# Optimization experiments

Measured on AMD Instinct MI355X. Metric: run time of the kernel, lower is better.

Reference implementation:

```python
import jax, jax.numpy as jnp
import numpy as np

N, C, H, M = 4096, 1024, 16, 4096
D = C // H
EPS = 1e-6


def rms_norm(x, g):
    # RMSNorm32: normalize in fp32 with eps=1e-6, affine scale g
    x32 = x.astype(jnp.float32)
    inv = jax.lax.rsqrt(jnp.mean(x32 * x32, axis=-1, keepdims=True) + EPS)
    return (x32 * inv).astype(x.dtype) * g


def setup_inputs() -> dict:
    key = jax.random.key(0)
    ks = jax.random.split(key, 6)
    s = 1.0 / np.sqrt(C)
    return {
        "x": jax.random.normal(ks[0], (N, C), jnp.float32),
        "g1": jnp.ones((C,), jnp.float32),
        "g2": jnp.ones((C,), jnp.float32),
        "w_qkv": jax.random.normal(ks[1], (C, 3 * C), jnp.float32) * s,
        "w_o": jax.random.normal(ks[2], (C, C), jnp.float32) * s,
        "w1": jax.random.normal(ks[3], (C, M), jnp.float32) * s,
        "w2": jax.random.normal(ks[4], (M, C), jnp.float32) * (1.0 / np.sqrt(M)),
    }


def reference(x, g1, g2, w_qkv, w_o, w1, w2):
    # --- pre-norm + full multi-head self-attention over all N sparse tokens ---
    h = rms_norm(x, g1)                                   # [N, C]
    qkv = (h @ w_qkv).reshape(N, 3, H, D)                 # [N, 3, H, D]
    q, k, v = qkv[:, 0], qkv[:, 1], qkv[:, 2]             # [N, H, D]
    scale = 1.0 / np.sqrt(D)
    scores = jnp.einsum('nhd,mhd->hnm', q, k) * scale     # [H, N, N]
    attn = jax.nn.softmax(scores, axis=-1)
    o = jnp.einsum('hnm,mhd->nhd', attn, v).reshape(N, C) # [N, C]
    x = x + o @ w_o                                       # residual
    # --- pre-norm + gated-free MLP (GELU tanh) ---
    h2 = rms_norm(x, g2)
    m = jax.nn.gelu(h2 @ w1, approximate=True) @ w2       # [N, C]
    return x + m
```

## Files before the change

### kernel.cpp

```cpp
#include <hip/hip_runtime.h>
#include <stdint.h>

#define TOK 4096
#define CH  1024
#define NH  16
#define HD  64
#define FF  4096

typedef __attribute__((ext_vector_type(8))) short bf16x8;
typedef __attribute__((ext_vector_type(4))) float f32x4;
typedef __attribute__((ext_vector_type(16))) float f32x16;

__device__ __forceinline__ unsigned short f2bf(float f) {
    union { float f; unsigned u; } v; v.f = f;
    unsigned u = v.u;
    u += 0x7fffu + ((u >> 16) & 1u);
    return (unsigned short)(u >> 16);
}

__device__ __forceinline__ unsigned cvtpk(float a, float b) {
    unsigned r;
    asm("v_cvt_pk_bf16_f32 %0, %1, %2" : "=v"(r) : "v"(a), "v"(b));
    return r;
}

__device__ __forceinline__ void load_lds16(const void* g, void* l) {
    __builtin_amdgcn_global_load_lds(
        (const __attribute__((address_space(1))) unsigned int*)g,
        (__attribute__((address_space(3))) unsigned int*)l, 16, 0, 0);
}

__device__ __forceinline__ float gelu_tanh(float u) {
    float z = 0.7978845608028654f * (u + 0.044715f * u * u * u);
    float e = __expf(2.0f * z);
    return 0.5f * u * (1.0f + (1.0f - 2.0f / (e + 1.0f)));
}

__global__ __launch_bounds__(256) void wT_kernel(const float* __restrict__ in,
                                                 unsigned short* __restrict__ out,
                                                 int K, int Nn) {
    __shared__ float tile[32][33];
    int k0 = blockIdx.x * 32, n0 = blockIdx.y * 32;
    int t = threadIdx.x, r = t >> 3, c = t & 7;
#pragma unroll
    for (int i = 0; i < 4; i++)
        tile[r][c + 8 * i] = in[(size_t)(k0 + r) * Nn + n0 + c + 8 * i];
    __syncthreads();
#pragma unroll
    for (int i = 0; i < 4; i++)
        out[(size_t)(n0 + r) * K + k0 + c + 8 * i] = f2bf(tile[c + 8 * i][r]);
}

__global__ __launch_bounds__(256) void rms_kernel(const float* __restrict__ x,
                                                  const float* __restrict__ g,
                                                  unsigned short* __restrict__ out) {
    int row = blockIdx.x, t = threadIdx.x;
    const float4* xr = (const float4*)(x + (size_t)row * CH);
    float4 v = xr[t];
    float ss = v.x * v.x + v.y * v.y + v.z * v.z + v.w * v.w;
#pragma unroll
    for (int m = 32; m; m >>= 1) ss += __shfl_xor(ss, m, 64);
    __shared__ float wsum[4];
    if ((t & 63) == 0) wsum[t >> 6] = ss;
    __syncthreads();
    float inv = rsqrtf((wsum[0] + wsum[1] + wsum[2] + wsum[3]) * (1.0f / CH) + 1e-6f);
    float4 gv = ((const float4*)g)[t];
    ushort4 o;
    o.x = f2bf(v.x * inv * gv.x);
    o.y = f2bf(v.y * inv * gv.y);
    o.z = f2bf(v.z * inv * gv.z);
    o.w = f2bf(v.w * inv * gv.w);
    ((ushort4*)(out + (size_t)row * CH))[t] = o;
}

template<int EPI>
__global__ __launch_bounds__(256) void gemm_bt(const unsigned short* __restrict__ A,
                                               const unsigned short* __restrict__ Bt,
                                               void* __restrict__ outp,
                                               const float* __restrict__ resid,
                                               int M, int Nn, int K) {
    __shared__ __align__(16) unsigned short lds[2][2][128 * 32];
    const int t = threadIdx.x, l = t & 63, w = t >> 6;
    const int nbn = Nn >> 7;
    const int bid = blockIdx.x, nwg = gridDim.x, cpx = nwg >> 3;
    const int swz = (bid & 7) * cpx + (bid >> 3);
    const int bm = swz / nbn, bn = swz % nbn;
    const int wr = w >> 1, wc = w & 1;
    const unsigned short* Ag = A + (size_t)bm * 128 * K;
    const unsigned short* Bg = Bt + (size_t)bn * 128 * K;

    f32x4 acc[4][4];
#pragma unroll
    for (int m = 0; m < 4; m++)
#pragma unroll
        for (int n = 0; n < 4; n++) acc[m][n] = {0.f, 0.f, 0.f, 0.f};

    auto stage = [&](int buf, int kt) {
#pragma unroll
        for (int p = 0; p < 2; p++) {
            int c = t + 256 * p;
            load_lds16(Ag + (size_t)(c >> 2) * K + kt * 32 + (c & 3) * 8, &lds[buf][0][c * 8]);
        }
#pragma unroll
        for (int p = 0; p < 2; p++) {
            int c = t + 256 * p;
            load_lds16(Bg + (size_t)(c >> 2) * K + kt * 32 + (c & 3) * 8, &lds[buf][1][c * 8]);
        }
    };

    stage(0, 0);
    __syncthreads();
    const int nkt = K >> 5;
    for (int kt = 0; kt < nkt; kt++) {
        const int buf = kt & 1;
        if (kt + 1 < nkt) stage(buf ^ 1, kt + 1);
        bf16x8 af[4], bfr[4];
#pragma unroll
        for (int m = 0; m < 4; m++)
            af[m] = *(const bf16x8*)&lds[buf][0][(wr * 64 + m * 16 + (l & 15)) * 32 + (l >> 4) * 8];
#pragma unroll
        for (int n = 0; n < 4; n++)
            bfr[n] = *(const bf16x8*)&lds[buf][1][(wc * 64 + n * 16 + (l & 15)) * 32 + (l >> 4) * 8];
#pragma unroll
        for (int m = 0; m < 4; m++)
#pragma unroll
            for (int n = 0; n < 4; n++)
                acc[m][n] = __builtin_amdgcn_mfma_f32_16x16x32_bf16(af[m], bfr[n], acc[m][n], 0, 0, 0);
        __syncthreads();
    }

    const int r0 = bm * 128 + wr * 64, c0 = bn * 128 + wc * 64;
#pragma unroll
    for (int m = 0; m < 4; m++)
#pragma unroll
        for (int n = 0; n < 4; n++)
#pragma unroll
            for (int r = 0; r < 4; r++) {
                int rr = r0 + m * 16 + (l >> 4) * 4 + r;
                int cc = c0 + n * 16 + (l & 15);
                float v = acc[m][n][r];
                if (EPI == 0) {
                    ((unsigned short*)outp)[(size_t)rr * Nn + cc] = f2bf(v);
                } else if (EPI == 1) {
                    ((unsigned short*)outp)[(size_t)rr * Nn + cc] = f2bf(gelu_tanh(v));
                } else if (EPI == 3) {
                    float sc = (cc < 1024) ? 0.180336880f : 1.0f;
                    ((unsigned short*)outp)[(size_t)rr * Nn + cc] = f2bf(v * sc);
                } else {
                    ((float*)outp)[(size_t)rr * Nn + cc] = resid[(size_t)rr * Nn + cc] + v;
                }
            }
}

__global__ __launch_bounds__(256) void vT_kernel(const unsigned short* __restrict__ qkv,
                                                 unsigned short* __restrict__ vT) {
    __shared__ unsigned short tile[64][80];
    const int t = threadIdx.x;
    const int t0 = blockIdx.x * 64;
    const int h = blockIdx.y;
#pragma unroll
    for (int p = 0; p < 2; p++) {
        int c = t + 256 * p;
        int r = c >> 3, c8 = (c & 7) * 8;
        bf16x8 v = *(const bf16x8*)(qkv + (size_t)(t0 + r) * 3072 + 2048 + h * 64 + c8);
        *(bf16x8*)&tile[r][c8] = v;
    }
    __syncthreads();
#pragma unroll
    for (int p = 0; p < 2; p++) {
        int c = t + 256 * p;
        int col = c >> 3, r8 = (c & 7) * 8;
        union { unsigned short u[8]; bf16x8 v; } o;
#pragma unroll
        for (int j = 0; j < 8; j++) o.u[j] = tile[r8 + j][col];
        *(bf16x8*)(vT + (size_t)(h * 64 + col) * 4096 + t0 + r8) = o.v;
    }
}

__global__ __launch_bounds__(256) void attn_kernel(const unsigned short* __restrict__ qkv,
                                                   const unsigned short* __restrict__ vT,
                                                   unsigned short* __restrict__ o) {
    __shared__ __align__(16) unsigned short Kl[2][4096];
    __shared__ __align__(16) unsigned short Vl[2][4096];
    const int t = threadIdx.x, l = t & 63, w = t >> 6;
    const int h = blockIdx.y;
    const int qrow = blockIdx.x * 128 + w * 32 + (l & 31);

    bf16x8 qf[4];
    {
        const unsigned short* qp = qkv + (size_t)qrow * 3072 + h * 64 + ((l >> 5) * 8);
#pragma unroll
        for (int c = 0; c < 4; c++) qf[c] = *(const bf16x8*)(qp + 16 * c);
    }
    const unsigned short* kb = qkv + 1024 + h * 64;
    const unsigned short* vb = vT + (size_t)h * 64 * 4096;

    int off8[4];
#pragma unroll
    for (int c = 0; c < 4; c++)
        off8[c] = (l & 31) * 64 + ((((l >> 5) + 2 * c) ^ (l & 7)) * 8);
    int kst[2], vst[2];
#pragma unroll
    for (int p = 0; p < 2; p++) {
        int c = t + 256 * p;
        int r = c >> 3, b = c & 7;
        kst[p] = r * 3072 + ((b ^ (r & 7)) * 8);
        vst[p] = r * 4096 + ((b ^ (r & 7)) * 8);
    }

    float lrun = 0.f;
    f32x16 accO[2];
#pragma unroll
    for (int dt = 0; dt < 2; dt++)
#pragma unroll
        for (int i = 0; i < 16; i++) accO[dt][i] = 0.f;

    auto stage = [&](int buf, int kt) {
#pragma unroll
        for (int p = 0; p < 2; p++)
            load_lds16(kb + (size_t)kt * 64 * 3072 + kst[p], &Kl[buf][(t + 256 * p) * 8]);
#pragma unroll
        for (int p = 0; p < 2; p++)
            load_lds16(vb + kt * 64 + vst[p], &Vl[buf][(t + 256 * p) * 8]);
    };

    stage(0, 0);
    __syncthreads();

    for (int kt = 0; kt < 64; kt++) {
        const int cur = kt & 1;
        if (kt + 1 < 64) stage(cur ^ 1, kt + 1);

        f32x16 s[2];
#pragma unroll
        for (int st = 0; st < 2; st++)
#pragma unroll
            for (int i = 0; i < 16; i++) s[st][i] = 0.f;

        __builtin_amdgcn_s_setprio(1);
#pragma unroll
        for (int st = 0; st < 2; st++)
#pragma unroll
            for (int c = 0; c < 4; c++) {
                bf16x8 kf = *(const bf16x8*)&Kl[cur][st * 2048 + off8[c]];
                s[st] = __builtin_amdgcn_mfma_f32_32x32x16_bf16(kf, qf[c], s[st], 0, 0, 0);
            }
        __builtin_amdgcn_s_setprio(0);

        float rs = 0.f;
#pragma unroll
        for (int st = 0; st < 2; st++)
#pragma unroll
            for (int i = 0; i < 16; i++) {
                float p = __builtin_amdgcn_exp2f(s[st][i]);
                s[st][i] = p;
                rs += p;
            }
        lrun += rs;

#pragma unroll
        for (int kc = 0; kc < 4; kc++) {
            const int base = 8 * (kc & 1);
            const f32x16& S = s[kc >> 1];
            unsigned w0 = cvtpk(S[base + 0], S[base + 1]);
            unsigned w1 = cvtpk(S[base + 2], S[base + 3]);
            unsigned w2 = cvtpk(S[base + 4], S[base + 5]);
            unsigned w3 = cvtpk(S[base + 6], S[base + 7]);
            asm("v_permlane32_swap_b32 %0, %1" : "+v"(w0), "+v"(w2));
            asm("v_permlane32_swap_b32 %0, %1" : "+v"(w1), "+v"(w3));
            union { unsigned u[4]; bf16x8 v; } pf;
            pf.u[0] = w0; pf.u[1] = w1; pf.u[2] = w2; pf.u[3] = w3;
            __builtin_amdgcn_s_setprio(1);
#pragma unroll
            for (int dt = 0; dt < 2; dt++) {
                bf16x8 vf = *(const bf16x8*)&Vl[cur][dt * 2048 + off8[kc]];
                accO[dt] = __builtin_amdgcn_mfma_f32_32x32x16_bf16(vf, pf.v, accO[dt], 0, 0, 0);
            }
            __builtin_amdgcn_s_setprio(0);
        }
        __syncthreads();
    }

    lrun += __shfl_xor(lrun, 32, 64);
    float inv = 1.0f / lrun;
    unsigned short* ob = o + (size_t)qrow * CH + h * 64 + 4 * (l >> 5);
#pragma unroll
    for (int dt = 0; dt < 2; dt++)
#pragma unroll
        for (int qd = 0; qd < 4; qd++) {
            ushort4 pk;
            pk.x = f2bf(accO[dt][qd * 4 + 0] * inv);
            pk.y = f2bf(accO[dt][qd * 4 + 1] * inv);
            pk.z = f2bf(accO[dt][qd * 4 + 2] * inv);
            pk.w = f2bf(accO[dt][qd * 4 + 3] * inv);
            *(ushort4*)(ob + dt * 32 + qd * 8) = pk;
        }
}

extern "C" void kernel_launch(void* const* d_in, const int* in_sizes, int n_in,
                              void* d_out, int out_size, void* d_ws, size_t ws_size,
                              hipStream_t stream) {
    const float* x     = (const float*)d_in[0];
    const float* g1    = (const float*)d_in[1];
    const float* g2    = (const float*)d_in[2];
    const float* w_qkv = (const float*)d_in[3];
    const float* w_o   = (const float*)d_in[4];
    const float* w1    = (const float*)d_in[5];
    const float* w2    = (const float*)d_in[6];

    char* ws = (char*)d_ws;
    unsigned short* wqkvT = (unsigned short*)(ws);
    unsigned short* woT   = (unsigned short*)(ws + 6291456);
    unsigned short* w1T   = (unsigned short*)(ws + 8388608);
    unsigned short* w2T   = (unsigned short*)(ws + 16777216);
    unsigned short* hbuf  = (unsigned short*)(ws + 25165824);
    unsigned short* qkv   = (unsigned short*)(ws + 33554432);
    unsigned short* obuf  = (unsigned short*)(ws + 58720256);
    float*          x2    = (float*)(ws + 67108864);
    unsigned short* abuf  = (unsigned short*)(ws + 83886080);
    unsigned short* vTb   = (unsigned short*)(ws + 83886080);

    dim3 b256(256);
    wT_kernel<<<dim3(CH / 32, 3 * CH / 32), b256, 0, stream>>>(w_qkv, wqkvT, CH, 3 * CH);
    wT_kernel<<<dim3(CH / 32, CH / 32),     b256, 0, stream>>>(w_o,   woT,   CH, CH);
    wT_kernel<<<dim3(CH / 32, FF / 32),     b256, 0, stream>>>(w1,    w1T,   CH, FF);
    wT_kernel<<<dim3(FF / 32, CH / 32),     b256, 0, stream>>>(w2,    w2T,   FF, CH);

    rms_kernel<<<TOK, b256, 0, stream>>>(x, g1, hbuf);
    gemm_bt<3><<<(TOK / 128) * (3 * CH / 128), b256, 0, stream>>>(hbuf, wqkvT, qkv, nullptr, TOK, 3 * CH, CH);
    vT_kernel<<<dim3(TOK / 64, NH), b256, 0, stream>>>(qkv, vTb);
    attn_kernel<<<dim3(TOK / 128, NH), b256, 0, stream>>>(qkv, vTb, obuf);
    gemm_bt<2><<<(TOK / 128) * (CH / 128), b256, 0, stream>>>(obuf, woT, x2, x, TOK, CH, CH);
    rms_kernel<<<TOK, b256, 0, stream>>>(x2, g2, hbuf);
    gemm_bt<1><<<(TOK / 128) * (FF / 128), b256, 0, stream>>>(hbuf, w1T, abuf, nullptr, TOK, FF, CH);
    gemm_bt<2><<<(TOK / 128) * (CH / 128), b256, 0, stream>>>(abuf, w2T, (float*)d_out, x2, TOK, CH, FF);
}
```

Baseline: 312.7 us.

## Split attention key range across wave pairs and read V fragments directly

The attention block now covers 64 queries instead of 128. Its four waves form two query halves times two key halves, each wave pair processing 32 of the 64 key tiles, and the partial outputs and row sums are merged through LDS at the end. This doubles the grid size, which helps occupancy and load balance. V is no longer staged in LDS; each wave loads its V fragments straight from global memory (transposed vT) into registers, removing the V LDS traffic. The cost is more global and L2 traffic for K and V per query, plus an extra reduction step.

```diff
diff --git a/kernel.cpp b/kernel.cpp
--- a/kernel.cpp
+++ b/kernel.cpp
@@ -180,11 +180,11 @@
 __global__ __launch_bounds__(256) void attn_kernel(const unsigned short* __restrict__ qkv,
                                                    const unsigned short* __restrict__ vT,
                                                    unsigned short* __restrict__ o) {
-    __shared__ __align__(16) unsigned short Kl[2][4096];
-    __shared__ __align__(16) unsigned short Vl[2][4096];
+    __shared__ __align__(16) unsigned short Kl[2][2][4096];
     const int t = threadIdx.x, l = t & 63, w = t >> 6;
     const int h = blockIdx.y;
-    const int qrow = blockIdx.x * 128 + w * 32 + (l & 31);
+    const int qhalf = w & 1, kthalf = w >> 1;
+    const int qrow = blockIdx.x * 64 + qhalf * 32 + (l & 31);
 
     bf16x8 qf[4];
     {
@@ -193,19 +193,19 @@
         for (int c = 0; c < 4; c++) qf[c] = *(const bf16x8*)(qp + 16 * c);
     }
     const unsigned short* kb = qkv + 1024 + h * 64;
-    const unsigned short* vb = vT + (size_t)h * 64 * 4096;
+    const unsigned short* vrow = vT + (size_t)(h * 64 + (l & 31)) * 4096 + (l >> 5) * 8;
 
     int off8[4];
 #pragma unroll
     for (int c = 0; c < 4; c++)
         off8[c] = (l & 31) * 64 + ((((l >> 5) + 2 * c) ^ (l & 7)) * 8);
-    int kst[2], vst[2];
-#pragma unroll
-    for (int p = 0; p < 2; p++) {
-        int c = t + 256 * p;
+    int kst[4], ldst[4];
+#pragma unroll
+    for (int p = 0; p < 4; p++) {
+        int c = qhalf * 64 + l + 128 * p;
         int r = c >> 3, b = c & 7;
         kst[p] = r * 3072 + ((b ^ (r & 7)) * 8);
-        vst[p] = r * 4096 + ((b ^ (r & 7)) * 8);
+        ldst[p] = c * 8;
     }
 
     float lrun = 0.f;
@@ -215,34 +215,32 @@
 #pragma unroll
         for (int i = 0; i < 16; i++) accO[dt][i] = 0.f;
 
-    auto stage = [&](int buf, int kt) {
-#pragma unroll
-        for (int p = 0; p < 2; p++)
-            load_lds16(kb + (size_t)kt * 64 * 3072 + kst[p], &Kl[buf][(t + 256 * p) * 8]);
-#pragma unroll
-        for (int p = 0; p < 2; p++)
-            load_lds16(vb + kt * 64 + vst[p], &Vl[buf][(t + 256 * p) * 8]);
+    auto stageK = [&](int buf, int ktg) {
+#pragma unroll
+        for (int p = 0; p < 4; p++)
+            load_lds16(kb + (size_t)ktg * 64 * 3072 + kst[p], &Kl[kthalf][buf][ldst[p]]);
     };
 
-    stage(0, 0);
-    __syncthreads();
-
-    for (int kt = 0; kt < 64; kt++) {
-        const int cur = kt & 1;
-        if (kt + 1 < 64) stage(cur ^ 1, kt + 1);
+    const int kt0 = kthalf * 32;
+    stageK(0, kt0);
+    __syncthreads();
+
+    for (int i = 0; i < 32; i++) {
+        const int cur = i & 1;
+        if (i + 1 < 32) stageK(cur ^ 1, kt0 + i + 1);
 
         f32x16 s[2];
 #pragma unroll
         for (int st = 0; st < 2; st++)
 #pragma unroll
-            for (int i = 0; i < 16; i++) s[st][i] = 0.f;
+            for (int j = 0; j < 16; j++) s[st][j] = 0.f;
 
         __builtin_amdgcn_s_setprio(1);
 #pragma unroll
         for (int st = 0; st < 2; st++)
 #pragma unroll
             for (int c = 0; c < 4; c++) {
-                bf16x8 kf = *(const bf16x8*)&Kl[cur][st * 2048 + off8[c]];
+                bf16x8 kf = *(const bf16x8*)&Kl[kthalf][cur][st * 2048 + off8[c]];
                 s[st] = __builtin_amdgcn_mfma_f32_32x32x16_bf16(kf, qf[c], s[st], 0, 0, 0);
             }
         __builtin_amdgcn_s_setprio(0);
@@ -251,13 +249,22 @@
 #pragma unroll
         for (int st = 0; st < 2; st++)
 #pragma unroll
-            for (int i = 0; i < 16; i++) {
-                float p = __builtin_amdgcn_exp2f(s[st][i]);
-                s[st][i] = p;
+            for (int j = 0; j < 16; j++) {
+                float p = __builtin_amdgcn_exp2f(s[st][j]);
+                s[st][j] = p;
                 rs += p;
             }
         lrun += rs;
 
+        const unsigned short* vk = vrow + (size_t)(kt0 + i) * 64;
+        bf16x8 vf[2][4];
+#pragma unroll
+        for (int dt = 0; dt < 2; dt++)
+#pragma unroll
+            for (int kc = 0; kc < 4; kc++)
+                vf[dt][kc] = *(const bf16x8*)(vk + dt * 32 * 4096 + kc * 16);
+
+        bf16x8 pf[4];
 #pragma unroll
         for (int kc = 0; kc < 4; kc++) {
             const int base = 8 * (kc & 1);
@@ -268,33 +275,53 @@
             unsigned w3 = cvtpk(S[base + 6], S[base + 7]);
             asm("v_permlane32_swap_b32 %0, %1" : "+v"(w0), "+v"(w2));
             asm("v_permlane32_swap_b32 %0, %1" : "+v"(w1), "+v"(w3));
-            union { unsigned u[4]; bf16x8 v; } pf;
-            pf.u[0] = w0; pf.u[1] = w1; pf.u[2] = w2; pf.u[3] = w3;
-            __builtin_amdgcn_s_setprio(1);
-#pragma unroll
-            for (int dt = 0; dt < 2; dt++) {
-                bf16x8 vf = *(const bf16x8*)&Vl[cur][dt * 2048 + off8[kc]];
-                accO[dt] = __builtin_amdgcn_mfma_f32_32x32x16_bf16(vf, pf.v, accO[dt], 0, 0, 0);
+            union { unsigned u[4]; bf16x8 v; } pu;
+            pu.u[0] = w0; pu.u[1] = w1; pu.u[2] = w2; pu.u[3] = w3;
+            pf[kc] = pu.v;
+        }
+
+        __builtin_amdgcn_s_setprio(1);
+#pragma unroll
+        for (int kc = 0; kc < 4; kc++)
+#pragma unroll
+            for (int dt = 0; dt < 2; dt++)
+                accO[dt] = __builtin_amdgcn_mfma_f32_32x32x16_bf16(vf[dt][kc], pf[kc], accO[dt], 0, 0, 0);
+        __builtin_amdgcn_s_setprio(0);
+        __syncthreads();
+    }
+
+    lrun += __shfl_xor(lrun, 32, 64);
+
+    float* xch = (float*)&Kl[0][0][0];
+    if (kthalf == 1) {
+        float* base = xch + (qhalf * 64 + l) * 33;
+#pragma unroll
+        for (int dt = 0; dt < 2; dt++)
+#pragma unroll
+            for (int i = 0; i < 16; i++) base[dt * 16 + i] = accO[dt][i];
+        base[32] = lrun;
+    }
+    __syncthreads();
+    if (kthalf == 0) {
+        const float* base = xch + (qhalf * 64 + l) * 33;
+#pragma unroll
+        for (int dt = 0; dt < 2; dt++)
+#pragma unroll
+            for (int i = 0; i < 16; i++) accO[dt][i] += base[dt * 16 + i];
+        float inv = 1.0f / (lrun + base[32]);
+        unsigned short* ob = o + (size_t)qrow * CH + h * 64 + 4 * (l >> 5);
+#pragma unroll
+        for (int dt = 0; dt < 2; dt++)
+#pragma unroll
+            for (int qd = 0; qd < 4; qd++) {
+                ushort4 pk;
+                pk.x = f2bf(accO[dt][qd * 4 + 0] * inv);
+                pk.y = f2bf(accO[dt][qd * 4 + 1] * inv);
+                pk.z = f2bf(accO[dt][qd * 4 + 2] * inv);
+                pk.w = f2bf(accO[dt][qd * 4 + 3] * inv);
+                *(ushort4*)(ob + dt * 32 + qd * 8) = pk;
             }
-            __builtin_amdgcn_s_setprio(0);
-        }
-        __syncthreads();
-    }
-
-    lrun += __shfl_xor(lrun, 32, 64);
-    float inv = 1.0f / lrun;
-    unsigned short* ob = o + (size_t)qrow * CH + h * 64 + 4 * (l >> 5);
-#pragma unroll
-    for (int dt = 0; dt < 2; dt++)
-#pragma unroll
-        for (int qd = 0; qd < 4; qd++) {
-            ushort4 pk;
-            pk.x = f2bf(accO[dt][qd * 4 + 0] * inv);
-            pk.y = f2bf(accO[dt][qd * 4 + 1] * inv);
-            pk.z = f2bf(accO[dt][qd * 4 + 2] * inv);
-            pk.w = f2bf(accO[dt][qd * 4 + 3] * inv);
-            *(ushort4*)(ob + dt * 32 + qd * 8) = pk;
-        }
+    }
 }
 
 extern "C" void kernel_launch(void* const* d_in, const int* in_sizes, int n_in,
@@ -329,7 +356,7 @@
     rms_kernel<<<TOK, b256, 0, stream>>>(x, g1, hbuf);
     gemm_bt<3><<<(TOK / 128) * (3 * CH / 128), b256, 0, stream>>>(hbuf, wqkvT, qkv, nullptr, TOK, 3 * CH, CH);
     vT_kernel<<<dim3(TOK / 64, NH), b256, 0, stream>>>(qkv, vTb);
-    attn_kernel<<<dim3(TOK / 128, NH), b256, 0, stream>>>(qkv, vTb, obuf);
+    attn_kernel<<<dim3(TOK / 64, NH), b256, 0, stream>>>(qkv, vTb, obuf);
     gemm_bt<2><<<(TOK / 128) * (CH / 128), b256, 0, stream>>>(obuf, woT, x2, x, TOK, CH, CH);
     rms_kernel<<<TOK, b256, 0, stream>>>(x2, g2, hbuf);
     gemm_bt<1><<<(TOK / 128) * (FF / 128), b256, 0, stream>>>(hbuf, w1T, abuf, nullptr, TOK, FF, CH);
```

Result: slower. 353.7 us (+13.1%).
